# Performance work log

Hardware: AMD Instinct MI355X
Metric: run time of the kernel (lower is better)

Reference implementation:

```python
import jax, jax.numpy as jnp
import numpy as np

N_HEADS = 12

def setup_inputs() -> dict:
    key = jax.random.key(0)
    ks = jax.random.split(key, 3)
    B, C, T = 4, 768, 2048
    x = jax.random.normal(ks[0], (B, C, T), dtype=jnp.float32)
    mask = jnp.ones((B, 1, 1, T), dtype=jnp.int32)  # all valid; masked_fill where mask==0
    Wqkv = jax.random.normal(ks[1], (3 * C, C), dtype=jnp.float32) * 0.02
    bqkv = jnp.zeros((3 * C,), dtype=jnp.float32)
    Wout = jax.random.normal(ks[2], (C, C), dtype=jnp.float32) * 0.02
    bout = jnp.zeros((C,), dtype=jnp.float32)
    return {"x": x, "mask": mask, "Wqkv": Wqkv, "bqkv": bqkv, "Wout": Wout, "bout": bout}


def reference(x, mask, Wqkv, bqkv, Wout, bout):
    B, C, T = x.shape
    H = N_HEADS
    d = C // H
    scale = 1.0 / jnp.sqrt(jnp.asarray(d, x.dtype))
    # 1x1 Conv1d == per-timestep matmul over channels
    qkv = jnp.einsum('oc,bct->bot', Wqkv, x) + bqkv[None, :, None]  # [B,3C,T]
    # channel dim splits as [3, H, d] per the torch view(B,3,H,d,T)
    qkv = qkv.reshape(B, 3, H, d, T).transpose(0, 1, 2, 4, 3)       # [B,3,H,T,d]
    q, k, v = qkv[:, 0], qkv[:, 1], qkv[:, 2]
    score = jnp.einsum('bhtd,bhsd->bhts', q, k) * scale             # [B,H,T,T]
    score = jnp.where(mask == 0, jnp.asarray(-10000.0, score.dtype), score)
    attn = jax.nn.softmax(score, axis=-1)  # dropout: eval mode (identity)
    o = jnp.einsum('bhts,bhsd->bhtd', attn, v)                      # [B,H,T,d]
    o = o.transpose(0, 1, 3, 2).reshape(B, C, T)                    # [B,C,T]
    return jnp.einsum('oc,bct->bot', Wout, o) + bout[None, :, None]
```

## Files before the change

kernel.cpp:

```cpp
#include <hip/hip_runtime.h>
#include <hip/hip_bf16.h>
#include <stdint.h>

#define B_   4
#define C_   768
#define T_   2048
#define H_   12
#define D_   64
#define O3_  2304

typedef __attribute__((ext_vector_type(4))) float f32x4;
typedef __attribute__((ext_vector_type(8))) short bf16x8;

__device__ __forceinline__ unsigned short f2bf(float f) {
  union { float f; unsigned int u; } v; v.f = f;
  unsigned int r = v.u + 0x7fffu + ((v.u >> 16) & 1u);
  return (unsigned short)(r >> 16);
}

__device__ __forceinline__ unsigned int pack2bf(float a, float b) {
  __hip_bfloat162 h2 = __float22bfloat162_rn(make_float2(a, b));
  union { __hip_bfloat162 h; unsigned int u; } cv; cv.h = h2;
  return cv.u;
}

__device__ __forceinline__ float fexp2(float x) {
#if __has_builtin(__builtin_amdgcn_exp2f)
  return __builtin_amdgcn_exp2f(x);
#else
  return exp2f(x);
#endif
}

__device__ __forceinline__ void async16(const void* g, void* lds) {
#if __has_builtin(__builtin_amdgcn_global_load_lds)
  __builtin_amdgcn_global_load_lds((const __attribute__((address_space(1))) void*)g,
                                   (__attribute__((address_space(3))) void*)lds, 16, 0, 0);
#else
  int lane = threadIdx.x & 63;
  *((uint4*)((char*)lds + lane * 16)) = *((const uint4*)g);
#endif
}


__global__ void cvt_f32_bf16(const float* __restrict__ in,
                             unsigned short* __restrict__ out, int n4) {
  int i = blockIdx.x * 256 + threadIdx.x;
  if (i < n4) {
    float4 f = ((const float4*)in)[i];
    ushort4 o;
    o.x = f2bf(f.x); o.y = f2bf(f.y); o.z = f2bf(f.z); o.w = f2bf(f.w);
    ((ushort4*)out)[i] = o;
  }
}

__global__ void make_bias(const int* __restrict__ mask, float* __restrict__ mbias, int n) {
  int i = blockIdx.x * 256 + threadIdx.x;
  if (i < n) mbias[i] = (mask[i] == 0) ? -14426.950408f : 0.0f;
}

__global__ void transpose_x(const float* __restrict__ x,
                            unsigned short* __restrict__ xT) {
  __shared__ unsigned short tile[32][33];
  int b = blockIdx.z;
  int c0 = blockIdx.y * 32;
  int t0 = blockIdx.x * 32;
  int tid = threadIdx.x;
  {
    int cl = tid >> 3;
    int tl = (tid & 7) * 4;
    float4 f = *(const float4*)(x + ((size_t)b * C_ + c0 + cl) * T_ + t0 + tl);
    tile[tl + 0][cl] = f2bf(f.x);
    tile[tl + 1][cl] = f2bf(f.y);
    tile[tl + 2][cl] = f2bf(f.z);
    tile[tl + 3][cl] = f2bf(f.w);
  }
  __syncthreads();
  {
    int tl = tid >> 3;
    int cl = (tid & 7) * 4;
    ushort4 o;
    o.x = tile[tl][cl + 0]; o.y = tile[tl][cl + 1];
    o.z = tile[tl][cl + 2]; o.w = tile[tl][cl + 3];
    *(ushort4*)(xT + ((size_t)b * T_ + t0 + tl) * C_ + c0 + cl) = o;
  }
}

__global__ __launch_bounds__(256)
void gemm_qkv(const unsigned short* __restrict__ xT,
              const unsigned short* __restrict__ W1,
              const float* __restrict__ bqkv,
              unsigned short* __restrict__ Qb,
              unsigned short* __restrict__ Kb,
              unsigned short* __restrict__ Vb) {
  __shared__ unsigned short sA[2][128 * 32];
  __shared__ unsigned short sB[2][128 * 32];

  const int b   = blockIdx.z;
  const int o0  = blockIdx.y * 128;
  const int t0  = blockIdx.x * 128;
  const int tid = threadIdx.x;
  const int wave = tid >> 6, lane = tid & 63;
  const int q = lane >> 4, ln = lane & 15;
  const int tw = wave >> 1, ow = wave & 1;

  const unsigned short* Ax = xT + (size_t)b * T_ * C_;
  const int srow = lane >> 2;
  const int scol = (lane & 3) * 8;

  const f32x4 ZERO = {0.f, 0.f, 0.f, 0.f};
  f32x4 acc[4][4];
#pragma unroll
  for (int mi = 0; mi < 4; ++mi)
#pragma unroll
    for (int ni = 0; ni < 4; ++ni) acc[mi][ni] = ZERO;

#pragma unroll
  for (int j = 0; j < 2; ++j) {
    const int chunk = wave * 2 + j;
    const int row = chunk * 16 + srow;
    async16(Ax + (size_t)(t0 + row) * C_ + scol, &sA[0][chunk * 512]);
    async16(W1 + (size_t)(o0 + row) * C_ + scol, &sB[0][chunk * 512]);
  }

  for (int i = 0; i < 24; ++i) {
    const int buf = i & 1;
    __syncthreads();
    if (i < 23) {
      const int k0 = (i + 1) * 32;
#pragma unroll
      for (int j = 0; j < 2; ++j) {
        const int chunk = wave * 2 + j;
        const int row = chunk * 16 + srow;
        async16(Ax + (size_t)(t0 + row) * C_ + k0 + scol, &sA[buf ^ 1][chunk * 512]);
        async16(W1 + (size_t)(o0 + row) * C_ + k0 + scol, &sB[buf ^ 1][chunk * 512]);
      }
    }

    bf16x8 aF[4], bF[4];
#pragma unroll
    for (int mi = 0; mi < 4; ++mi)
      aF[mi] = *(const bf16x8*)(&sA[buf][(tw * 64 + mi * 16 + ln) * 32 + q * 8]);
#pragma unroll
    for (int ni = 0; ni < 4; ++ni)
      bF[ni] = *(const bf16x8*)(&sB[buf][(ow * 64 + ni * 16 + ln) * 32 + q * 8]);
#pragma unroll
    for (int mi = 0; mi < 4; ++mi)
#pragma unroll
      for (int ni = 0; ni < 4; ++ni)
        acc[mi][ni] = __builtin_amdgcn_mfma_f32_16x16x32_bf16(aF[mi], bF[ni], acc[mi][ni], 0, 0, 0);
  }

  const float QSCL = 0.125f * 1.44269504f;
#pragma unroll
  for (int ni = 0; ni < 4; ++ni) {
    const int o = o0 + ow * 64 + ni * 16 + ln;
    const float bias = bqkv[o];
    const int which = o / C_;
    const int rem = o - which * C_;
    const int bh = b * H_ + (rem >> 6);
    const int dd = rem & 63;
#pragma unroll
    for (int mi = 0; mi < 4; ++mi) {
      const int tb = t0 + tw * 64 + mi * 16 + q * 4;
      f32x4 v = acc[mi][ni];
      if (which == 0) {
#pragma unroll
        for (int r = 0; r < 4; ++r)
          Qb[((size_t)bh * T_ + tb + r) * D_ + dd] = f2bf((v[r] + bias) * QSCL);
      } else if (which == 1) {
#pragma unroll
        for (int r = 0; r < 4; ++r) {
          const int s = tb + r;
          const int cp = (dd >> 3) ^ (s & 7);
          Kb[((size_t)bh * T_ + s) * 64 + (cp << 3) + (dd & 7)] = f2bf(v[r] + bias);
        }
      } else {
        const int tile = tb >> 6, si = tb & 63;
        const int cp = (si >> 3) ^ (dd & 7);
        ushort4 pk;
        pk.x = f2bf(v[0] + bias);
        pk.y = f2bf(v[1] + bias);
        pk.z = f2bf(v[2] + bias);
        pk.w = f2bf(v[3] + bias);
        *(ushort4*)(Vb + (((size_t)bh * 32 + tile) * 64 + dd) * 64 + (cp << 3) + (si & 7)) = pk;
      }
    }
  }
}

__global__ __launch_bounds__(256, 3)
void attn(const unsigned short* __restrict__ Qb,
          const unsigned short* __restrict__ Kb,
          const unsigned short* __restrict__ Vb,
          const float* __restrict__ mbias,
          unsigned short* __restrict__ Ob) {
  __shared__ __align__(16) char smem[49152];
  unsigned short* sK0 = (unsigned short*)smem;
  unsigned short* sV0 = (unsigned short*)(smem + 24576);

  const int id = blockIdx.x;
  const int bh = id % 48;
  const int tblk = id / 48;
  const int b = bh / H_, h = bh % H_;
  const int tid = threadIdx.x, wave = tid >> 6, lane = tid & 63;
  const int q = lane >> 4, ln = lane & 15;
  const int t0w = tblk * 128 + wave * 32;

  bf16x8 Qa[2][2];
#pragma unroll
  for (int tt = 0; tt < 2; ++tt) {
    const unsigned short* qrow = Qb + ((size_t)bh * T_ + t0w + tt * 16 + ln) * D_;
    Qa[tt][0] = *(const bf16x8*)(qrow + q * 8);
    Qa[tt][1] = *(const bf16x8*)(qrow + 32 + q * 8);
  }

  const f32x4 ZERO = {0.f, 0.f, 0.f, 0.f};
  f32x4 Oacc[4][2];
  f32x4 lacc[2];
#pragma unroll
  for (int dt = 0; dt < 4; ++dt)
#pragma unroll
    for (int tt = 0; tt < 2; ++tt) Oacc[dt][tt] = ZERO;
#pragma unroll
  for (int tt = 0; tt < 2; ++tt) lacc[tt] = ZERO;

  const short one_s = (ln == 0) ? (short)0x3F80 : (short)0;
  bf16x8 ones;
#pragma unroll
  for (int j = 0; j < 8; ++j) ones[j] = one_s;

  const unsigned short* gK = Kb + (size_t)bh * T_ * 64;
  const unsigned short* gV = Vb + (size_t)bh * 32 * 4096;
  const float* mb = mbias + b * T_;

  unsigned int maskbits = 0;
  for (int t2 = 0; t2 < 32; ++t2)
    if (__ballot(mb[t2 * 64 + lane] != 0.0f) != 0ull) maskbits |= (1u << t2);

  auto stage = [&](const unsigned short* g, unsigned short* lds) {
#pragma unroll
    for (int j = 0; j < 2; ++j) {
      const int chunk = wave * 2 + j;
      async16(g + chunk * 512 + lane * 8, lds + chunk * 512);
    }
  };

  auto sync4 = [&]() {
    __builtin_amdgcn_sched_barrier(0);
    asm volatile("s_waitcnt vmcnt(4) lgkmcnt(0)" ::: "memory");
    __builtin_amdgcn_s_barrier();
    __builtin_amdgcn_sched_barrier(0);
  };
  auto sync0 = [&]() {
    __builtin_amdgcn_sched_barrier(0);
    asm volatile("s_waitcnt vmcnt(0) lgkmcnt(0)" ::: "memory");
    __builtin_amdgcn_s_barrier();
    __builtin_amdgcn_sched_barrier(0);
  };

  auto QK = [&](const unsigned short* sKc, int it, bf16x8 pfO[2][2]) {
    const int s0 = it * 64;
    const bool anymask = (maskbits >> it) & 1;
#pragma unroll
    for (int kc = 0; kc < 2; ++kc) {
      bf16x8 kf0[2], kf1[2];
#pragma unroll
      for (int sb = 0; sb < 2; ++sb) {
        const unsigned short* krow = sKc + (kc * 32 + sb * 16 + ln) * 64;
        kf0[sb] = *(const bf16x8*)(krow + ((q ^ (ln & 7)) << 3));
        kf1[sb] = *(const bf16x8*)(krow + (((4 + q) ^ (ln & 7)) << 3));
      }
#pragma unroll
      for (int tt = 0; tt < 2; ++tt) {
        f32x4 sc[2];
#pragma unroll
        for (int sb = 0; sb < 2; ++sb) {
          f32x4 p0 = __builtin_amdgcn_mfma_f32_16x16x32_bf16(kf0[sb], Qa[tt][0], ZERO, 0, 0, 0);
          sc[sb]   = __builtin_amdgcn_mfma_f32_16x16x32_bf16(kf1[sb], Qa[tt][1], p0, 0, 0, 0);
          if (anymask) {
            f32x4 bb = *(const f32x4*)(mb + s0 + kc * 32 + sb * 16 + q * 4);
#pragma unroll
            for (int r = 0; r < 4; ++r) sc[sb][r] += bb[r];
          }
        }
        unsigned int A0 = pack2bf(fexp2(sc[0][0]), fexp2(sc[0][1]));
        unsigned int B0 = pack2bf(fexp2(sc[0][2]), fexp2(sc[0][3]));
        unsigned int C0 = pack2bf(fexp2(sc[1][0]), fexp2(sc[1][1]));
        unsigned int E0 = pack2bf(fexp2(sc[1][2]), fexp2(sc[1][3]));
        asm volatile("v_permlane32_swap_b32 %0, %1" : "+v"(A0), "+v"(C0));
        asm volatile("v_permlane16_swap_b32 %0, %1" : "+v"(A0), "+v"(C0));
        asm volatile("v_permlane32_swap_b32 %0, %1" : "+v"(B0), "+v"(E0));
        asm volatile("v_permlane16_swap_b32 %0, %1" : "+v"(B0), "+v"(E0));
        union { bf16x8 v; unsigned int u[4]; } P;
        P.u[0] = A0;
        P.u[1] = B0;
        P.u[2] = C0;
        P.u[3] = E0;
        pfO[tt][kc] = P.v;
      }
    }
  };

  auto PV = [&](const unsigned short* sVc, bf16x8 pfI[2][2]) {
#pragma unroll
    for (int dt = 0; dt < 4; ++dt) {
#pragma unroll
      for (int kc = 0; kc < 2; ++kc) {
        bf16x8 vf = *(const bf16x8*)(sVc + (dt * 16 + ln) * 64 +
                                     (((kc * 4 + q) ^ (ln & 7)) << 3));
#pragma unroll
        for (int tt = 0; tt < 2; ++tt)
          Oacc[dt][tt] = __builtin_amdgcn_mfma_f32_16x16x32_bf16(vf, pfI[tt][kc], Oacc[dt][tt], 0, 0, 0);
      }
    }
#pragma unroll
    for (int kc = 0; kc < 2; ++kc)
#pragma unroll
      for (int tt = 0; tt < 2; ++tt)
        lacc[tt] = __builtin_amdgcn_mfma_f32_16x16x32_bf16(ones, pfI[tt][kc], lacc[tt], 0, 0, 0);
  };

  bf16x8 pf[2][2];

  stage(gK, sK0);
  stage(gV, sV0);
  stage(gK + 4096, sK0 + 4096);
  stage(gV + 4096, sV0 + 4096);

  for (int ith = 0; ith < 10; ++ith) {
    const int it = ith * 3;
    sync4();
    stage(gK + (size_t)(it + 2) * 4096, sK0 + 2 * 4096);
    stage(gV + (size_t)(it + 2) * 4096, sV0 + 2 * 4096);
    QK(sK0, it, pf);
    PV(sV0, pf);
    sync4();
    stage(gK + (size_t)(it + 3) * 4096, sK0);
    stage(gV + (size_t)(it + 3) * 4096, sV0);
    QK(sK0 + 4096, it + 1, pf);
    PV(sV0 + 4096, pf);
    sync4();
    stage(gK + (size_t)(it + 4) * 4096, sK0 + 4096);
    stage(gV + (size_t)(it + 4) * 4096, sV0 + 4096);
    QK(sK0 + 2 * 4096, it + 2, pf);
    PV(sV0 + 2 * 4096, pf);
  }

  sync4();
  QK(sK0, 30, pf);
  PV(sV0, pf);
  sync0();
  QK(sK0 + 4096, 31, pf);
  PV(sV0 + 4096, pf);

#pragma unroll
  for (int tt = 0; tt < 2; ++tt) {
    const float lv = __shfl(lacc[tt][0], ln, 64);
    const float inv = 1.0f / lv;
    const int t = t0w + tt * 16 + ln;
#pragma unroll
    for (int dt = 0; dt < 4; ++dt) {
      f32x4 o = Oacc[dt][tt];
      ushort4 pk;
      pk.x = f2bf(o[0] * inv);
      pk.y = f2bf(o[1] * inv);
      pk.z = f2bf(o[2] * inv);
      pk.w = f2bf(o[3] * inv);
      *(ushort4*)(Ob + ((size_t)b * T_ + t) * C_ + h * D_ + dt * 16 + q * 4) = pk;
    }
  }
}

__global__ __launch_bounds__(256)
void gemm_out(const unsigned short* __restrict__ Ob,
              const unsigned short* __restrict__ W2,
              const float* __restrict__ bout,
              float* __restrict__ out) {
  __shared__ unsigned short sA[2][128 * 32];
  __shared__ unsigned short sB[2][128 * 32];

  const int b   = blockIdx.z;
  const int o0  = blockIdx.y * 128;
  const int t0  = blockIdx.x * 128;
  const int tid = threadIdx.x;
  const int wave = tid >> 6, lane = tid & 63;
  const int q = lane >> 4, ln = lane & 15;
  const int tw = wave >> 1, ow = wave & 1;

  const unsigned short* Bo = Ob + (size_t)b * T_ * C_;
  const int srow = lane >> 2;
  const int scol = (lane & 3) * 8;

  const f32x4 ZERO = {0.f, 0.f, 0.f, 0.f};
  f32x4 acc[4][4];
#pragma unroll
  for (int mi = 0; mi < 4; ++mi)
#pragma unroll
    for (int ni = 0; ni < 4; ++ni) acc[mi][ni] = ZERO;

#pragma unroll
  for (int j = 0; j < 2; ++j) {
    const int chunk = wave * 2 + j;
    const int row = chunk * 16 + srow;
    async16(W2 + (size_t)(o0 + row) * C_ + scol, &sA[0][chunk * 512]);
    async16(Bo + (size_t)(t0 + row) * C_ + scol, &sB[0][chunk * 512]);
  }

  for (int i = 0; i < 24; ++i) {
    const int buf = i & 1;
    __syncthreads();
    if (i < 23) {
      const int k0 = (i + 1) * 32;
#pragma unroll
      for (int j = 0; j < 2; ++j) {
        const int chunk = wave * 2 + j;
        const int row = chunk * 16 + srow;
        async16(W2 + (size_t)(o0 + row) * C_ + k0 + scol, &sA[buf ^ 1][chunk * 512]);
        async16(Bo + (size_t)(t0 + row) * C_ + k0 + scol, &sB[buf ^ 1][chunk * 512]);
      }
    }

    bf16x8 aF[4], bF[4];
#pragma unroll
    for (int mi = 0; mi < 4; ++mi)
      aF[mi] = *(const bf16x8*)(&sA[buf][(tw * 64 + mi * 16 + ln) * 32 + q * 8]);
#pragma unroll
    for (int ni = 0; ni < 4; ++ni)
      bF[ni] = *(const bf16x8*)(&sB[buf][(ow * 64 + ni * 16 + ln) * 32 + q * 8]);
#pragma unroll
    for (int mi = 0; mi < 4; ++mi)
#pragma unroll
      for (int ni = 0; ni < 4; ++ni)
        acc[mi][ni] = __builtin_amdgcn_mfma_f32_16x16x32_bf16(aF[mi], bF[ni], acc[mi][ni], 0, 0, 0);
  }

#pragma unroll
  for (int mi = 0; mi < 4; ++mi) {
    const int ob = o0 + tw * 64 + mi * 16 + q * 4;
#pragma unroll
    for (int ni = 0; ni < 4; ++ni) {
      const int t = t0 + ow * 64 + ni * 16 + ln;
      f32x4 v = acc[mi][ni];
#pragma unroll
      for (int r = 0; r < 4; ++r)
        out[((size_t)b * C_ + ob + r) * T_ + t] = v[r] + bout[ob + r];
    }
  }
}


extern "C" void kernel_launch(void* const* d_in, const int* in_sizes, int n_in,
                              void* d_out, int out_size, void* d_ws, size_t ws_size,
                              hipStream_t stream) {
  (void)in_sizes; (void)n_in; (void)out_size; (void)ws_size;
  const float* x    = (const float*)d_in[0];
  const int*   mask = (const int*)d_in[1];
  const float* Wqkv = (const float*)d_in[2];
  const float* bqkv = (const float*)d_in[3];
  const float* Wout = (const float*)d_in[4];
  const float* bout = (const float*)d_in[5];
  float* out = (float*)d_out;

  const size_t szHead = (size_t)B_ * H_ * T_ * D_;
  const size_t szBTC  = (size_t)B_ * T_ * C_;
  unsigned short* Qb  = (unsigned short*)d_ws;
  unsigned short* Kb  = Qb + szHead;
  unsigned short* Vb  = Kb + szHead;
  unsigned short* Ob  = Vb + szHead;
  unsigned short* xT  = Ob + szBTC;
  unsigned short* W1b = xT + szBTC;
  unsigned short* W2b = W1b + (size_t)O3_ * C_;
  float* mbias        = (float*)(W2b + (size_t)C_ * C_);

  cvt_f32_bf16<<<dim3((O3_ * C_ / 4 + 255) / 256), 256, 0, stream>>>(Wqkv, W1b, O3_ * C_ / 4);
  cvt_f32_bf16<<<dim3((C_ * C_ / 4 + 255) / 256), 256, 0, stream>>>(Wout, W2b, C_ * C_ / 4);
  make_bias<<<dim3((B_ * T_ + 255) / 256), 256, 0, stream>>>(mask, mbias, B_ * T_);
  transpose_x<<<dim3(T_ / 32, C_ / 32, B_), 256, 0, stream>>>(x, xT);
  gemm_qkv<<<dim3(T_ / 128, O3_ / 128, B_), 256, 0, stream>>>(xT, W1b, bqkv, Qb, Kb, Vb);
  attn<<<dim3(768), 256, 0, stream>>>(Qb, Kb, Vb, mbias, Ob);
  gemm_out<<<dim3(T_ / 128, C_ / 128, B_), 256, 0, stream>>>(Ob, W2b, bout, out);
}
```

Baseline: 227.9 us.

## Triple-buffer GEMM LDS staging with swizzled layout and explicit waitcnt barriers

Both projection GEMMs move from a double-buffered to a triple-buffered async LDS pipeline. Explicit vmcnt-based waits let two K-tiles stay in flight while the current one is computed. The LDS column layout is XOR-swizzled to cut bank conflicts on fragment reads. This raises LDS use per block to 48KB and adds an occupancy hint of 3 blocks, at the cost of more LDS pressure and hand-coded waitcnt counts that must match the number of issued loads.

Result: no change. 225.1 us (-1.3%).

```diff
diff --git a/kernel.cpp b/kernel.cpp
--- a/kernel.cpp
+++ b/kernel.cpp
@@ -86,15 +86,15 @@
   }
 }
 
-__global__ __launch_bounds__(256)
+__global__ __launch_bounds__(256, 3)
 void gemm_qkv(const unsigned short* __restrict__ xT,
               const unsigned short* __restrict__ W1,
               const float* __restrict__ bqkv,
               unsigned short* __restrict__ Qb,
               unsigned short* __restrict__ Kb,
               unsigned short* __restrict__ Vb) {
-  __shared__ unsigned short sA[2][128 * 32];
-  __shared__ unsigned short sB[2][128 * 32];
+  __shared__ unsigned short sA[3][128 * 32];
+  __shared__ unsigned short sB[3][128 * 32];
 
   const int b   = blockIdx.z;
   const int o0  = blockIdx.y * 128;
@@ -106,7 +106,9 @@
 
   const unsigned short* Ax = xT + (size_t)b * T_ * C_;
   const int srow = lane >> 2;
-  const int scol = (lane & 3) * 8;
+  const int ssw  = ((lane >> 2) ^ (lane >> 4)) & 3;
+  const int scol = ((lane & 3) ^ ssw) * 8;
+  const int rsw  = (ln ^ (ln >> 2)) & 3;
 
   const f32x4 ZERO = {0.f, 0.f, 0.f, 0.f};
   f32x4 acc[4][4];
@@ -115,41 +117,61 @@
 #pragma unroll
     for (int ni = 0; ni < 4; ++ni) acc[mi][ni] = ZERO;
 
-#pragma unroll
-  for (int j = 0; j < 2; ++j) {
-    const int chunk = wave * 2 + j;
-    const int row = chunk * 16 + srow;
-    async16(Ax + (size_t)(t0 + row) * C_ + scol, &sA[0][chunk * 512]);
-    async16(W1 + (size_t)(o0 + row) * C_ + scol, &sB[0][chunk * 512]);
-  }
-
-  for (int i = 0; i < 24; ++i) {
-    const int buf = i & 1;
-    __syncthreads();
-    if (i < 23) {
-      const int k0 = (i + 1) * 32;
-#pragma unroll
-      for (int j = 0; j < 2; ++j) {
-        const int chunk = wave * 2 + j;
-        const int row = chunk * 16 + srow;
-        async16(Ax + (size_t)(t0 + row) * C_ + k0 + scol, &sA[buf ^ 1][chunk * 512]);
-        async16(W1 + (size_t)(o0 + row) * C_ + k0 + scol, &sB[buf ^ 1][chunk * 512]);
-      }
-    }
-
+  auto stageA = [&](int ks, int bufi) {
+#pragma unroll
+    for (int j = 0; j < 2; ++j) {
+      const int chunk = wave * 2 + j;
+      async16(Ax + (size_t)(t0 + chunk * 16 + srow) * C_ + ks * 32 + scol,
+              &sA[bufi][chunk * 512]);
+    }
+  };
+  auto stageB = [&](int ks, int bufi) {
+#pragma unroll
+    for (int j = 0; j < 2; ++j) {
+      const int chunk = wave * 2 + j;
+      async16(W1 + (size_t)(o0 + chunk * 16 + srow) * C_ + ks * 32 + scol,
+              &sB[bufi][chunk * 512]);
+    }
+  };
+  auto sync4 = [&]() {
+    __builtin_amdgcn_sched_barrier(0);
+    asm volatile("s_waitcnt vmcnt(4) lgkmcnt(0)" ::: "memory");
+    __builtin_amdgcn_s_barrier();
+    __builtin_amdgcn_sched_barrier(0);
+  };
+  auto sync0 = [&]() {
+    __builtin_amdgcn_sched_barrier(0);
+    asm volatile("s_waitcnt vmcnt(0) lgkmcnt(0)" ::: "memory");
+    __builtin_amdgcn_s_barrier();
+    __builtin_amdgcn_sched_barrier(0);
+  };
+  auto compute = [&](int bufi) {
     bf16x8 aF[4], bF[4];
 #pragma unroll
     for (int mi = 0; mi < 4; ++mi)
-      aF[mi] = *(const bf16x8*)(&sA[buf][(tw * 64 + mi * 16 + ln) * 32 + q * 8]);
+      aF[mi] = *(const bf16x8*)(&sA[bufi][(tw * 64 + mi * 16 + ln) * 32 + ((q ^ rsw) << 3)]);
 #pragma unroll
     for (int ni = 0; ni < 4; ++ni)
-      bF[ni] = *(const bf16x8*)(&sB[buf][(ow * 64 + ni * 16 + ln) * 32 + q * 8]);
+      bF[ni] = *(const bf16x8*)(&sB[bufi][(ow * 64 + ni * 16 + ln) * 32 + ((q ^ rsw) << 3)]);
 #pragma unroll
     for (int mi = 0; mi < 4; ++mi)
 #pragma unroll
       for (int ni = 0; ni < 4; ++ni)
         acc[mi][ni] = __builtin_amdgcn_mfma_f32_16x16x32_bf16(aF[mi], bF[ni], acc[mi][ni], 0, 0, 0);
-  }
+  };
+
+  stageA(0, 0); stageB(0, 0);
+  stageA(1, 1); stageB(1, 1);
+
+  for (int g = 0; g < 7; ++g) {
+    const int t3 = g * 3;
+    sync4(); stageA(t3 + 2, 2); stageB(t3 + 2, 2); compute(0);
+    sync4(); stageA(t3 + 3, 0); stageB(t3 + 3, 0); compute(1);
+    sync4(); stageA(t3 + 4, 1); stageB(t3 + 4, 1); compute(2);
+  }
+  sync4(); stageA(23, 2); stageB(23, 2); compute(0);
+  sync4(); compute(1);
+  sync0(); compute(2);
 
   const float QSCL = 0.125f * 1.44269504f;
 #pragma unroll
@@ -372,13 +394,13 @@
   }
 }
 
-__global__ __launch_bounds__(256)
+__global__ __launch_bounds__(256, 3)
 void gemm_out(const unsigned short* __restrict__ Ob,
               const unsigned short* __restrict__ W2,
               const float* __restrict__ bout,
               float* __restrict__ out) {
-  __shared__ unsigned short sA[2][128 * 32];
-  __shared__ unsigned short sB[2][128 * 32];
+  __shared__ unsigned short sA[3][128 * 32];
+  __shared__ unsigned short sB[3][128 * 32];
 
   const int b   = blockIdx.z;
   const int o0  = blockIdx.y * 128;
@@ -390,7 +412,9 @@
 
   const unsigned short* Bo = Ob + (size_t)b * T_ * C_;
   const int srow = lane >> 2;
-  const int scol = (lane & 3) * 8;
+  const int ssw  = ((lane >> 2) ^ (lane >> 4)) & 3;
+  const int scol = ((lane & 3) ^ ssw) * 8;
+  const int rsw  = (ln ^ (ln >> 2)) & 3;
 
   const f32x4 ZERO = {0.f, 0.f, 0.f, 0.f};
   f32x4 acc[4][4];
@@ -399,41 +423,61 @@
 #pragma unroll
     for (int ni = 0; ni < 4; ++ni) acc[mi][ni] = ZERO;
 
-#pragma unroll
-  for (int j = 0; j < 2; ++j) {
-    const int chunk = wave * 2 + j;
-    const int row = chunk * 16 + srow;
-    async16(W2 + (size_t)(o0 + row) * C_ + scol, &sA[0][chunk * 512]);
-    async16(Bo + (size_t)(t0 + row) * C_ + scol, &sB[0][chunk * 512]);
-  }
-
-  for (int i = 0; i < 24; ++i) {
-    const int buf = i & 1;
-    __syncthreads();
-    if (i < 23) {
-      const int k0 = (i + 1) * 32;
-#pragma unroll
-      for (int j = 0; j < 2; ++j) {
-        const int chunk = wave * 2 + j;
-        const int row = chunk * 16 + srow;
-        async16(W2 + (size_t)(o0 + row) * C_ + k0 + scol, &sA[buf ^ 1][chunk * 512]);
-        async16(Bo + (size_t)(t0 + row) * C_ + k0 + scol, &sB[buf ^ 1][chunk * 512]);
-      }
-    }
-
+  auto stageA = [&](int ks, int bufi) {
+#pragma unroll
+    for (int j = 0; j < 2; ++j) {
+      const int chunk = wave * 2 + j;
+      async16(W2 + (size_t)(o0 + chunk * 16 + srow) * C_ + ks * 32 + scol,
+              &sA[bufi][chunk * 512]);
+    }
+  };
+  auto stageB = [&](int ks, int bufi) {
+#pragma unroll
+    for (int j = 0; j < 2; ++j) {
+      const int chunk = wave * 2 + j;
+      async16(Bo + (size_t)(t0 + chunk * 16 + srow) * C_ + ks * 32 + scol,
+              &sB[bufi][chunk * 512]);
+    }
+  };
+  auto sync4 = [&]() {
+    __builtin_amdgcn_sched_barrier(0);
+    asm volatile("s_waitcnt vmcnt(4) lgkmcnt(0)" ::: "memory");
+    __builtin_amdgcn_s_barrier();
+    __builtin_amdgcn_sched_barrier(0);
+  };
+  auto sync0 = [&]() {
+    __builtin_amdgcn_sched_barrier(0);
+    asm volatile("s_waitcnt vmcnt(0) lgkmcnt(0)" ::: "memory");
+    __builtin_amdgcn_s_barrier();
+    __builtin_amdgcn_sched_barrier(0);
+  };
+  auto compute = [&](int bufi) {
     bf16x8 aF[4], bF[4];
 #pragma unroll
     for (int mi = 0; mi < 4; ++mi)
-      aF[mi] = *(const bf16x8*)(&sA[buf][(tw * 64 + mi * 16 + ln) * 32 + q * 8]);
+      aF[mi] = *(const bf16x8*)(&sA[bufi][(tw * 64 + mi * 16 + ln) * 32 + ((q ^ rsw) << 3)]);
 #pragma unroll
     for (int ni = 0; ni < 4; ++ni)
-      bF[ni] = *(const bf16x8*)(&sB[buf][(ow * 64 + ni * 16 + ln) * 32 + q * 8]);
+      bF[ni] = *(const bf16x8*)(&sB[bufi][(ow * 64 + ni * 16 + ln) * 32 + ((q ^ rsw) << 3)]);
 #pragma unroll
     for (int mi = 0; mi < 4; ++mi)
 #pragma unroll
       for (int ni = 0; ni < 4; ++ni)
         acc[mi][ni] = __builtin_amdgcn_mfma_f32_16x16x32_bf16(aF[mi], bF[ni], acc[mi][ni], 0, 0, 0);
-  }
+  };
+
+  stageA(0, 0); stageB(0, 0);
+  stageA(1, 1); stageB(1, 1);
+
+  for (int g = 0; g < 7; ++g) {
+    const int t3 = g * 3;
+    sync4(); stageA(t3 + 2, 2); stageB(t3 + 2, 2); compute(0);
+    sync4(); stageA(t3 + 3, 0); stageB(t3 + 3, 0); compute(1);
+    sync4(); stageA(t3 + 4, 1); stageB(t3 + 4, 1); compute(2);
+  }
+  sync4(); stageA(23, 2); stageB(23, 2); compute(0);
+  sync4(); compute(1);
+  sync0(); compute(2);
 
 #pragma unroll
   for (int mi = 0; mi < 4; ++mi) {
```
